# Performance work log

Measured on AMD Instinct MI355X. Metric: run time of the kernel, lower is better.

Reference implementation:

```python
import jax, jax.numpy as jnp
import numpy as np

N, G, E, F, H = 65536, 32768, 600000, 128, 128

def _mlp(x, w1, b1, w2, b2):
    # Linear -> SiLU -> Linear
    return jax.nn.silu(x @ w1 + b1) @ w2 + b2

def setup_inputs() -> dict:
    key = jax.random.key(0)
    ks = jax.random.split(key, 24)
    def lin(k, din, dout):
        kw, kb = jax.random.split(k)
        s = 1.0 / np.sqrt(din)
        return (jax.random.uniform(kw, (din, dout), jnp.float32, -s, s),
                jax.random.uniform(kb, (dout,), jnp.float32, -s, s))
    nm_w1, nm_b1 = lin(ks[0], F, H)
    nm_w2, nm_b2 = lin(ks[1], H, H)
    em_w1, em_b1 = lin(ks[2], 6, H)
    em_w2, em_b2 = lin(ks[3], H, H)
    mm_w1, mm_b1 = lin(ks[4], 2 * H, H)
    mm_w2, mm_b2 = lin(ks[5], H, H)
    um_w1, um_b1 = lin(ks[6], H, H)
    um_w2, um_b2 = lin(ks[7], H, H)
    return {
        "node_features": jax.random.normal(ks[8], (N, F), jnp.float32),
        "node_pos": jax.random.uniform(ks[9], (N, 3), jnp.float32),
        "grid_pos": jax.random.uniform(ks[10], (G, 3), jnp.float32),
        "edge_index": jax.random.randint(ks[11], (2, E), 0, G, jnp.int64),
        "nm_w1": nm_w1, "nm_b1": nm_b1, "nm_w2": nm_w2, "nm_b2": nm_b2,
        "em_w1": em_w1, "em_b1": em_b1, "em_w2": em_w2, "em_b2": em_b2,
        "mm_w1": mm_w1, "mm_b1": mm_b1, "mm_w2": mm_w2, "mm_b2": mm_b2,
        "um_w1": um_w1, "um_b1": um_b1, "um_w2": um_w2, "um_b2": um_b2,
    }

def reference(node_features, node_pos, grid_pos, edge_index,
              nm_w1, nm_b1, nm_w2, nm_b2,
              em_w1, em_b1, em_w2, em_b2,
              mm_w1, mm_b1, mm_w2, mm_b2,
              um_w1, um_b1, um_w2, um_b2):
    src, tgt = edge_index[0], edge_index[1]
    # node_model on all points [N,H]
    nf = _mlp(node_features, nm_w1, nm_b1, nm_w2, nm_b2)
    # edge features from gathered positions [E,6] -> [E,H]
    edge_attr = jnp.concatenate([node_pos[src], grid_pos[tgt]], axis=-1)
    ef = _mlp(edge_attr, em_w1, em_b1, em_w2, em_b2)
    # messages [E,2H] -> [E,H]
    msg = _mlp(jnp.concatenate([nf[src], ef], axis=-1), mm_w1, mm_b1, mm_w2, mm_b2)
    # scatter-add mean aggregation to grid [G,H]
    counts = jax.ops.segment_sum(jnp.ones((msg.shape[0],), msg.dtype), tgt, num_segments=G)
    counts = jnp.maximum(counts, 1.0)[:, None]
    agg = jax.ops.segment_sum(msg, tgt, num_segments=G) / counts
    # update_model [G,H]
    return _mlp(agg, um_w1, um_b1, um_w2, um_b2)
```

## Files before the change

kernel.cpp:

```cpp
#include <hip/hip_runtime.h>

#define N_NODES 65536
#define G_GRID  32768
#define E_EDGES 600000
#define HD      128

typedef __attribute__((ext_vector_type(8))) short bf8;
typedef __attribute__((ext_vector_type(4))) float f32x4;

__device__ __forceinline__ short f2bf(float f){
  union { float f; unsigned u; } v; v.f = f;
  unsigned r = v.u + 0x7FFFu + ((v.u >> 16) & 1u);
  return (short)(r >> 16);
}

__device__ __forceinline__ bf8 load_pack8(const float* p, float scale){
  float4 u0 = *(const float4*)p;
  float4 u1 = *(const float4*)(p + 4);
  bf8 r;
  r[0]=f2bf(u0.x*scale); r[1]=f2bf(u0.y*scale); r[2]=f2bf(u0.z*scale); r[3]=f2bf(u0.w*scale);
  r[4]=f2bf(u1.x*scale); r[5]=f2bf(u1.y*scale); r[6]=f2bf(u1.z*scale); r[7]=f2bf(u1.w*scale);
  return r;
}

__global__ void prep_w_k(const float* __restrict__ nmw1, const float* __restrict__ nmw2,
                         const float* __restrict__ emw2, const float* __restrict__ mmw1,
                         const float* __restrict__ mmw2, const float* __restrict__ umw1,
                         const float* __restrict__ umw2, short* __restrict__ dst)
{
  int i = blockIdx.x*256 + threadIdx.x;
  const float* src; int local; bool k256 = false;
  if      (i < 16384){ src = nmw1; local = i; }
  else if (i < 32768){ src = nmw2; local = i - 16384; }
  else if (i < 49152){ src = emw2; local = i - 32768; }
  else if (i < 81920){ src = mmw1; local = i - 49152; k256 = true; }
  else if (i < 98304){ src = mmw2; local = i - 81920; }
  else if (i < 114688){ src = umw1; local = i - 98304; }
  else               { src = umw2; local = i - 114688; }
  int n, k;
  if (k256){ n = local >> 8; k = local & 255; }
  else     { n = local >> 7; k = local & 127; }
  dst[i] = f2bf(src[k*HD + n]);
}

__global__ void prep_combo_k(const float* __restrict__ emw1, const float* __restrict__ eb1,
                             const float* __restrict__ emw2, const float* __restrict__ eb2,
                             const float* __restrict__ mmw1, const float* __restrict__ mb1,
                             short* __restrict__ wcombot, float* __restrict__ bcombo,
                             float* __restrict__ ew1c)
{
  int gid = blockIdx.x*256 + threadIdx.x;
  if (gid < 16384){
    int k = gid >> 7, n = gid & 127;
    float a0 = 0.f, a1 = 0.f;
    #pragma unroll 4
    for (int j=0;j<HD;j+=2){
      a0 += emw2[k*HD + j]     * mmw1[(HD + j)*HD + n];
      a1 += emw2[k*HD + j + 1] * mmw1[(HD + j + 1)*HD + n];
    }
    wcombot[n*HD + k] = f2bf(a0 + a1);
  } else if (gid < 16512){
    int n = gid - 16384;
    float acc = mb1[n];
    for (int j=0;j<HD;j++) acc += eb2[j] * mmw1[(HD + j)*HD + n];
    bcombo[n] = acc;
  } else if (gid < 16640){
    int n = gid - 16512;
    #pragma unroll
    for (int k=0;k<6;k++) ew1c[n*8 + k] = emw1[k*HD + n];
    ew1c[n*8 + 6] = eb1[n];
    ew1c[n*8 + 7] = 0.f;
  }
}

__global__ void node_mlp_k(const float* __restrict__ X,
                           const short* __restrict__ w1t, const float* __restrict__ b1,
                           const short* __restrict__ w2t, const float* __restrict__ b2,
                           short* __restrict__ nf)
{
  __shared__ short hid[64][136];
  const int t = threadIdx.x;
  const int wave = t >> 6, lane = t & 63, l15 = lane & 15, q = lane >> 4;
  const int rw = blockIdx.x*64 + wave*16;

  bf8 a[4];
  const float* xr = X + (size_t)(rw + l15)*HD;
  #pragma unroll
  for (int kt=0; kt<4; kt++) a[kt] = load_pack8(xr + kt*32 + q*8, 1.0f);

  #pragma unroll
  for (int ct=0; ct<8; ct++){
    f32x4 acc = {0.f,0.f,0.f,0.f};
    #pragma unroll
    for (int kt=0; kt<4; kt++){
      bf8 b = *(const bf8*)(w1t + (ct*16 + l15)*HD + kt*32 + q*8);
      acc = __builtin_amdgcn_mfma_f32_16x16x32_bf16(a[kt], b, acc, 0, 0, 0);
    }
    float bias = b1[ct*16 + l15];
    #pragma unroll
    for (int r=0;r<4;r++){
      float v = acc[r] + bias;
      v = v / (1.f + __expf(-v));
      hid[wave*16 + q*4 + r][ct*16 + l15] = f2bf(v);
    }
  }
  bf8 a2[4];
  #pragma unroll
  for (int kt=0;kt<4;kt++) a2[kt] = *(const bf8*)&hid[wave*16 + l15][kt*32 + q*8];
  #pragma unroll
  for (int ct=0; ct<8; ct++){
    f32x4 acc = {0.f,0.f,0.f,0.f};
    #pragma unroll
    for (int kt=0;kt<4;kt++){
      bf8 b = *(const bf8*)(w2t + (ct*16 + l15)*HD + kt*32 + q*8);
      acc = __builtin_amdgcn_mfma_f32_16x16x32_bf16(a2[kt], b, acc, 0, 0, 0);
    }
    float bias = b2[ct*16 + l15];
    #pragma unroll
    for (int r=0;r<4;r++)
      nf[(size_t)(rw + q*4 + r)*HD + ct*16 + l15] = f2bf(acc[r] + bias);
  }
}

__global__ void count_k(const int* __restrict__ eidx, int* __restrict__ counts){
  int e = blockIdx.x*256 + threadIdx.x;
  if (e < E_EDGES) atomicAdd(&counts[eidx[E_EDGES + e]], 1);
}

__global__ void scan_k(const int* __restrict__ counts, int* __restrict__ offs){
  __shared__ int part[1024];
  const int t = threadIdx.x;
  const int base = t*32;
  int loc[32];
  int s = 0;
  #pragma unroll
  for (int i=0;i<32;i++){ loc[i] = s; s += counts[base+i]; }
  part[t] = s;
  __syncthreads();
  for (int off=1; off<1024; off<<=1){
    int v = (t>=off) ? part[t-off] : 0;
    __syncthreads();
    part[t] += v;
    __syncthreads();
  }
  int pre = (t==0) ? 0 : part[t-1];
  #pragma unroll
  for (int i=0;i<32;i++) offs[base+i] = pre + loc[i];
  if (t==1023) offs[G_GRID] = pre + s;
}

__global__ void scatter_k(const int* __restrict__ eidx, const int* __restrict__ offs,
                          int* __restrict__ counts,
                          int* __restrict__ srcs_s, int* __restrict__ tgts_s){
  int e = blockIdx.x*256 + threadIdx.x;
  if (e < E_EDGES){
    int g = eidx[E_EDGES + e];
    int slot = offs[g] + atomicSub(&counts[g], 1) - 1;
    srcs_s[slot] = eidx[e];
    tgts_s[slot] = g;
  }
}

__global__ void __launch_bounds__(256, 3)
edge_msg5_k(const int* __restrict__ srcs_s, const int* __restrict__ tgts_s,
            const float* __restrict__ npos, const float* __restrict__ gpos,
            const float* __restrict__ ew1c_g, const float* __restrict__ bcombo,
            const short* __restrict__ mw1t, const short* __restrict__ wcombot,
            const short* __restrict__ mw2t, const float* __restrict__ mb2,
            const short* __restrict__ nf, float* __restrict__ agg)
{
  __shared__ float ew1l[128][8];
  __shared__ int tgtl[128];
  __shared__ short hm[128][136];

  const int t = threadIdx.x;
  const int e0 = blockIdx.x*128;
  const int w = t >> 6, lane = t & 63, l15 = lane & 15, q = lane >> 4;
  const int base = e0 + w*32;

  int i0 = base + l15;      if (i0 >= E_EDGES) i0 = E_EDGES - 1;
  int i1 = base + 16 + l15; if (i1 >= E_EDGES) i1 = E_EDGES - 1;
  int s0 = srcs_s[i0], s1 = srcs_s[i1];
  int g0 = tgts_s[i0], g1 = tgts_s[i1];

  bf8 an0[4], an1[4];
  {
    const short* n0p = nf + (size_t)s0*HD + q*8;
    const short* n1p = nf + (size_t)s1*HD + q*8;
    #pragma unroll
    for (int kt=0;kt<4;kt++){ an0[kt] = *(const bf8*)(n0p + kt*32); an1[kt] = *(const bf8*)(n1p + kt*32); }
  }
  float a0=npos[s0*3+0], a1=npos[s0*3+1], a2=npos[s0*3+2];
  float a3=gpos[g0*3+0], a4=gpos[g0*3+1], a5=gpos[g0*3+2];
  float b0=npos[s1*3+0], b1=npos[s1*3+1], b2=npos[s1*3+2];
  float b3=gpos[g1*3+0], b4=gpos[g1*3+1], b5=gpos[g1*3+2];

  if (t < 128){
    int idx = e0 + t; if (idx >= E_EDGES) idx = E_EDGES - 1;
    tgtl[t] = tgts_s[idx];
    *(f32x4*)&ew1l[t][0] = *(const f32x4*)&ew1c_g[t*8];
    *(f32x4*)&ew1l[t][4] = *(const f32x4*)&ew1c_g[t*8 + 4];
  }
  __syncthreads();

  {
    int r0 = w*32 + l15, r1 = r0 + 16;
    #pragma unroll
    for (int pg=0; pg<4; pg++){
      bf8 pk0, pk1;
      #pragma unroll
      for (int j=0;j<8;j++){
        int n = q*32 + pg*8 + j;
        f32x4 wa = *(const f32x4*)&ew1l[n][0];
        f32x4 wb = *(const f32x4*)&ew1l[n][4];
        float v0 = wb[2] + a0*wa[0] + a1*wa[1] + a2*wa[2] + a3*wa[3] + a4*wb[0] + a5*wb[1];
        v0 = v0 / (1.f + __expf(-v0));
        pk0[j] = f2bf(v0);
        float v1 = wb[2] + b0*wa[0] + b1*wa[1] + b2*wa[2] + b3*wa[3] + b4*wb[0] + b5*wb[1];
        v1 = v1 / (1.f + __expf(-v1));
        pk1[j] = f2bf(v1);
      }
      *(bf8*)&hm[r0][q*32 + pg*8] = pk0;
      *(bf8*)&hm[r1][q*32 + pg*8] = pk1;
    }
  }

  bf8 ah0[4], ah1[4];
  #pragma unroll
  for (int kt=0;kt<4;kt++){
    ah0[kt] = *(const bf8*)&hm[w*32 + l15][kt*32 + q*8];
    ah1[kt] = *(const bf8*)&hm[w*32 + 16 + l15][kt*32 + q*8];
  }
  #pragma unroll
  for (int ct=0; ct<8; ct++){
    bf8 bw1[4], bwc[4];
    #pragma unroll
    for (int kt=0;kt<4;kt++){
      bw1[kt] = *(const bf8*)(mw1t + (ct*16 + l15)*256 + kt*32 + q*8);
      bwc[kt] = *(const bf8*)(wcombot + (ct*16 + l15)*HD + kt*32 + q*8);
    }
    f32x4 acc0 = {0.f,0.f,0.f,0.f}, acc1 = {0.f,0.f,0.f,0.f};
    #pragma unroll
    for (int kt=0;kt<4;kt++){
      acc0 = __builtin_amdgcn_mfma_f32_16x16x32_bf16(an0[kt], bw1[kt], acc0, 0,0,0);
      acc1 = __builtin_amdgcn_mfma_f32_16x16x32_bf16(an1[kt], bw1[kt], acc1, 0,0,0);
    }
    #pragma unroll
    for (int kt=0;kt<4;kt++){
      acc0 = __builtin_amdgcn_mfma_f32_16x16x32_bf16(ah0[kt], bwc[kt], acc0, 0,0,0);
      acc1 = __builtin_amdgcn_mfma_f32_16x16x32_bf16(ah1[kt], bwc[kt], acc1, 0,0,0);
    }
    float bias = bcombo[ct*16 + l15];
    int col = ct*16 + l15;
    #pragma unroll
    for (int r=0;r<4;r++){
      float v0 = acc0[r] + bias;
      v0 = v0 / (1.f + __expf(-v0));
      hm[w*32 + q*4 + r][col] = f2bf(v0);
      float v1 = acc1[r] + bias;
      v1 = v1 / (1.f + __expf(-v1));
      hm[w*32 + 16 + q*4 + r][col] = f2bf(v1);
    }
  }

  bf8 am0[4], am1[4];
  #pragma unroll
  for (int kt=0;kt<4;kt++){
    am0[kt] = *(const bf8*)&hm[w*32 + l15][kt*32 + q*8];
    am1[kt] = *(const bf8*)&hm[w*32 + 16 + l15][kt*32 + q*8];
  }

  float* msgf_w = (float*)&hm[w*32][0];
  int lim0 = E_EDGES - base;      if (lim0 > 16) lim0 = 16;
  int lim1 = E_EDGES - base - 16; if (lim1 > 16) lim1 = 16;
  int c2 = lane*2;
  int cur = -1; float sx = 0.f, sy = 0.f;

  #pragma unroll
  for (int ct=0; ct<8; ct++){
    f32x4 acc = {0.f,0.f,0.f,0.f};
    #pragma unroll
    for (int kt=0;kt<4;kt++){
      bf8 b = *(const bf8*)(mw2t + (ct*16 + l15)*HD + kt*32 + q*8);
      acc = __builtin_amdgcn_mfma_f32_16x16x32_bf16(am0[kt], b, acc, 0,0,0);
    }
    float bias = mb2[ct*16 + l15];
    int col = ct*16 + l15;
    #pragma unroll
    for (int r=0;r<4;r++) msgf_w[(q*4 + r)*132 + col] = acc[r] + bias;
  }
  if (lim0 > 0){
    cur = tgtl[w*32];
    for (int r=0; r<lim0; r++){
      int tg = tgtl[w*32 + r];
      float2 v = *(const float2*)&msgf_w[r*132 + c2];
      if (tg != cur){
        atomicAdd(&agg[(size_t)cur*HD + c2], sx);
        atomicAdd(&agg[(size_t)cur*HD + c2 + 1], sy);
        cur = tg; sx = v.x; sy = v.y;
      } else { sx += v.x; sy += v.y; }
    }
  }

  if (lim1 > 0){
    #pragma unroll
    for (int ct=0; ct<8; ct++){
      f32x4 acc = {0.f,0.f,0.f,0.f};
      #pragma unroll
      for (int kt=0;kt<4;kt++){
        bf8 b = *(const bf8*)(mw2t + (ct*16 + l15)*HD + kt*32 + q*8);
        acc = __builtin_amdgcn_mfma_f32_16x16x32_bf16(am1[kt], b, acc, 0,0,0);
      }
      float bias = mb2[ct*16 + l15];
      int col = ct*16 + l15;
      #pragma unroll
      for (int r=0;r<4;r++) msgf_w[(q*4 + r)*132 + col] = acc[r] + bias;
    }
    for (int r=0; r<lim1; r++){
      int tg = tgtl[w*32 + 16 + r];
      float2 v = *(const float2*)&msgf_w[r*132 + c2];
      if (tg != cur){
        atomicAdd(&agg[(size_t)cur*HD + c2], sx);
        atomicAdd(&agg[(size_t)cur*HD + c2 + 1], sy);
        cur = tg; sx = v.x; sy = v.y;
      } else { sx += v.x; sy += v.y; }
    }
  }
  if (cur >= 0){
    atomicAdd(&agg[(size_t)cur*HD + c2], sx);
    atomicAdd(&agg[(size_t)cur*HD + c2 + 1], sy);
  }
}

__global__ void update_mlp2_k(const float* __restrict__ agg, const int* __restrict__ offs,
                              const short* __restrict__ w1t, const float* __restrict__ b1,
                              const short* __restrict__ w2t, const float* __restrict__ b2,
                              float* __restrict__ out)
{
  __shared__ short hid[64][136];
  const int t = threadIdx.x;
  const int wave = t >> 6, lane = t & 63, l15 = lane & 15, q = lane >> 4;
  const int rw = blockIdx.x*64 + wave*16;

  int row = rw + l15;
  float c = (float)(offs[row+1] - offs[row]);
  float rcp = 1.0f / fmaxf(c, 1.0f);
  bf8 a[4];
  const float* ar = agg + (size_t)row*HD;
  #pragma unroll
  for (int kt=0; kt<4; kt++) a[kt] = load_pack8(ar + kt*32 + q*8, rcp);

  #pragma unroll
  for (int ct=0; ct<8; ct++){
    f32x4 acc = {0.f,0.f,0.f,0.f};
    #pragma unroll
    for (int kt=0; kt<4; kt++){
      bf8 b = *(const bf8*)(w1t + (ct*16 + l15)*HD + kt*32 + q*8);
      acc = __builtin_amdgcn_mfma_f32_16x16x32_bf16(a[kt], b, acc, 0, 0, 0);
    }
    float bias = b1[ct*16 + l15];
    #pragma unroll
    for (int r=0;r<4;r++){
      float v = acc[r] + bias;
      v = v / (1.f + __expf(-v));
      hid[wave*16 + q*4 + r][ct*16 + l15] = f2bf(v);
    }
  }
  bf8 a2[4];
  #pragma unroll
  for (int kt=0;kt<4;kt++) a2[kt] = *(const bf8*)&hid[wave*16 + l15][kt*32 + q*8];
  #pragma unroll
  for (int ct=0; ct<8; ct++){
    f32x4 acc = {0.f,0.f,0.f,0.f};
    #pragma unroll
    for (int kt=0;kt<4;kt++){
      bf8 b = *(const bf8*)(w2t + (ct*16 + l15)*HD + kt*32 + q*8);
      acc = __builtin_amdgcn_mfma_f32_16x16x32_bf16(a2[kt], b, acc, 0, 0, 0);
    }
    float bias = b2[ct*16 + l15];
    #pragma unroll
    for (int r=0;r<4;r++)
      out[(size_t)(rw + q*4 + r)*HD + ct*16 + l15] = acc[r] + bias;
  }
}

extern "C" void kernel_launch(void* const* d_in, const int* in_sizes, int n_in,
                              void* d_out, int out_size, void* d_ws, size_t ws_size,
                              hipStream_t stream)
{
  const float* node_features = (const float*)d_in[0];
  const float* node_pos      = (const float*)d_in[1];
  const float* grid_pos      = (const float*)d_in[2];
  const int*   edge_index    = (const int*)d_in[3];
  const float* nm_w1 = (const float*)d_in[4];
  const float* nm_b1 = (const float*)d_in[5];
  const float* nm_w2 = (const float*)d_in[6];
  const float* nm_b2 = (const float*)d_in[7];
  const float* em_w1 = (const float*)d_in[8];
  const float* em_b1 = (const float*)d_in[9];
  const float* em_w2 = (const float*)d_in[10];
  const float* em_b2 = (const float*)d_in[11];
  const float* mm_w1 = (const float*)d_in[12];
  const float* mm_b1 = (const float*)d_in[13];
  const float* mm_w2 = (const float*)d_in[14];
  const float* mm_b2 = (const float*)d_in[15];
  const float* um_w1 = (const float*)d_in[16];
  const float* um_b1 = (const float*)d_in[17];
  const float* um_w2 = (const float*)d_in[18];
  const float* um_b2 = (const float*)d_in[19];
  float* out = (float*)d_out;

  char* ws = (char*)d_ws;
  short* nf     = (short*)ws;
  int*   counts = (int*)  (ws + 16777216ull);
  int*   offs   = (int*)  (ws + 16908288ull);
  short* wts    = (short*)(ws + 17039424ull);
  short* wcombot= (short*)(ws + 17301568ull);
  float* bcombo = (float*)(ws + 17334336ull);
  float* ew1c   = (float*)(ws + 17334848ull);
  int*   srcs_s = (int*)  (ws + 17338944ull);
  int*   tgts_s = (int*)  (ws + 19738944ull);

  short* nmw1t = wts;
  short* nmw2t = wts + 16384;
  short* mmw1t = wts + 49152;
  short* mmw2t = wts + 81920;
  short* umw1t = wts + 98304;
  short* umw2t = wts + 114688;

  float* agg = out;

  (void)hipMemsetAsync(counts, 0, 131072, stream);
  (void)hipMemsetAsync(out, 0, (size_t)G_GRID*HD*4, stream);

  prep_w_k<<<512, 256, 0, stream>>>(nm_w1, nm_w2, em_w2, mm_w1, mm_w2, um_w1, um_w2, wts);
  prep_combo_k<<<65, 256, 0, stream>>>(em_w1, em_b1, em_w2, em_b2, mm_w1, mm_b1,
                                       wcombot, bcombo, ew1c);
  node_mlp_k<<<G_GRID/64, 256, 0, stream>>>(node_features, nmw1t, nm_b1, nmw2t, nm_b2, nf);
  count_k<<<(E_EDGES+255)/256, 256, 0, stream>>>(edge_index, counts);
  scan_k<<<1, 1024, 0, stream>>>(counts, offs);
  scatter_k<<<(E_EDGES+255)/256, 256, 0, stream>>>(edge_index, offs, counts, srcs_s, tgts_s);
  edge_msg5_k<<<(E_EDGES + 127)/128, 256, 0, stream>>>(srcs_s, tgts_s, node_pos, grid_pos,
      ew1c, bcombo, mmw1t, wcombot, mmw2t, mm_b2, nf, agg);
  update_mlp2_k<<<G_GRID/64, 256, 0, stream>>>(agg, offs, umw1t, um_b1, umw2t, um_b2, out);
}
```

Baseline: 538.7 us.

## Compute edge-MLP first layer with split-bf16 MFMA instead of scalar FMAs

The 6-input first edge-MLP layer now runs on MFMA instead of per-lane scalar FMA loops over an LDS weight table. Inputs and weights are split into hi/lo bf16 parts and packed into a K=32 fragment with a constant-one bias column, so fp32 accuracy is roughly kept (hi*hi + lo*hi + hi*lo terms). This removes the LDS weight staging and a block-wide barrier. The weight-combination prep kernel is also split across more blocks with a two-half reduction. The cost is extra packing work per edge and a more scattered write pattern into the shared hidden tile.

```diff
diff --git a/kernel.cpp b/kernel.cpp
--- a/kernel.cpp
+++ b/kernel.cpp
@@ -12,6 +12,9 @@
   union { float f; unsigned u; } v; v.f = f;
   unsigned r = v.u + 0x7FFFu + ((v.u >> 16) & 1u);
   return (short)(r >> 16);
+}
+__device__ __forceinline__ float bf2f(short s){
+  union { unsigned u; float f; } v; v.u = ((unsigned)(unsigned short)s) << 16; return v.f;
 }
 
 __device__ __forceinline__ bf8 load_pack8(const float* p, float scale){
@@ -43,33 +46,46 @@
   dst[i] = f2bf(src[k*HD + n]);
 }
 
-__global__ void prep_combo_k(const float* __restrict__ emw1, const float* __restrict__ eb1,
-                             const float* __restrict__ emw2, const float* __restrict__ eb2,
-                             const float* __restrict__ mmw1, const float* __restrict__ mb1,
-                             short* __restrict__ wcombot, float* __restrict__ bcombo,
-                             float* __restrict__ ew1c)
-{
-  int gid = blockIdx.x*256 + threadIdx.x;
-  if (gid < 16384){
-    int k = gid >> 7, n = gid & 127;
-    float a0 = 0.f, a1 = 0.f;
-    #pragma unroll 4
-    for (int j=0;j<HD;j+=2){
-      a0 += emw2[k*HD + j]     * mmw1[(HD + j)*HD + n];
-      a1 += emw2[k*HD + j + 1] * mmw1[(HD + j + 1)*HD + n];
-    }
-    wcombot[n*HD + k] = f2bf(a0 + a1);
-  } else if (gid < 16512){
-    int n = gid - 16384;
-    float acc = mb1[n];
-    for (int j=0;j<HD;j++) acc += eb2[j] * mmw1[(HD + j)*HD + n];
-    bcombo[n] = acc;
-  } else if (gid < 16640){
-    int n = gid - 16512;
-    #pragma unroll
-    for (int k=0;k<6;k++) ew1c[n*8 + k] = emw1[k*HD + n];
-    ew1c[n*8 + 6] = eb1[n];
-    ew1c[n*8 + 7] = 0.f;
+__global__ void prep_combo2_k(const float* __restrict__ emw1, const float* __restrict__ eb1,
+                              const float* __restrict__ emw2, const float* __restrict__ eb2,
+                              const float* __restrict__ mmw1, const float* __restrict__ mb1,
+                              short* __restrict__ wcombot, float* __restrict__ bcombo,
+                              short* __restrict__ ew1x)
+{
+  if (blockIdx.x < 128){
+    __shared__ float part[2][128];
+    int k = blockIdx.x;
+    int t = threadIdx.x, n = t & 127, half = t >> 7;
+    float acc = 0.f;
+    const float* er = emw2 + k*HD + half*64;
+    #pragma unroll 8
+    for (int j=0;j<64;j++) acc += er[j] * mmw1[(HD + half*64 + j)*HD + n];
+    part[half][n] = acc;
+    __syncthreads();
+    if (half == 0) wcombot[n*HD + k] = f2bf(part[0][n] + part[1][n]);
+  } else {
+    int t = threadIdx.x;
+    if (t < 128){
+      int n = t;
+      float acc = mb1[n];
+      for (int j=0;j<HD;j++) acc += eb2[j] * mmw1[(HD + j)*HD + n];
+      bcombo[n] = acc;
+      short v[32];
+      #pragma unroll
+      for (int i=0;i<32;i++) v[i] = 0;
+      #pragma unroll
+      for (int i=0;i<6;i++){
+        float wv = emw1[i*HD + n];
+        short wh = f2bf(wv);
+        short wl = f2bf(wv - bf2f(wh));
+        v[i] = wh; v[6+i] = wh; v[12+i] = wl;
+      }
+      float bv = eb1[n];
+      short bh = f2bf(bv);
+      v[18] = bh; v[19] = f2bf(bv - bf2f(bh));
+      #pragma unroll
+      for (int i=0;i<32;i++) ew1x[n*32 + i] = v[i];
+    }
   }
 }
 
@@ -161,15 +177,34 @@
   }
 }
 
+__device__ __forceinline__ bf8 build_af(const float p[6], int q){
+  short ph[6], pl[6];
+  #pragma unroll
+  for (int i=0;i<6;i++){
+    ph[i] = f2bf(p[i]);
+    pl[i] = f2bf(p[i] - bf2f(ph[i]));
+  }
+  bf8 af = {0,0,0,0,0,0,0,0};
+  if (q == 0){
+    af[0]=ph[0]; af[1]=ph[1]; af[2]=ph[2]; af[3]=ph[3];
+    af[4]=ph[4]; af[5]=ph[5]; af[6]=pl[0]; af[7]=pl[1];
+  } else if (q == 1){
+    af[0]=pl[2]; af[1]=pl[3]; af[2]=pl[4]; af[3]=pl[5];
+    af[4]=ph[0]; af[5]=ph[1]; af[6]=ph[2]; af[7]=ph[3];
+  } else if (q == 2){
+    af[0]=ph[4]; af[1]=ph[5]; af[2]=(short)0x3F80; af[3]=(short)0x3F80;
+  }
+  return af;
+}
+
 __global__ void __launch_bounds__(256, 3)
-edge_msg5_k(const int* __restrict__ srcs_s, const int* __restrict__ tgts_s,
+edge_msg6_k(const int* __restrict__ srcs_s, const int* __restrict__ tgts_s,
             const float* __restrict__ npos, const float* __restrict__ gpos,
-            const float* __restrict__ ew1c_g, const float* __restrict__ bcombo,
+            const short* __restrict__ ew1x, const float* __restrict__ bcombo,
             const short* __restrict__ mw1t, const short* __restrict__ wcombot,
             const short* __restrict__ mw2t, const float* __restrict__ mb2,
             const short* __restrict__ nf, float* __restrict__ agg)
 {
-  __shared__ float ew1l[128][8];
   __shared__ int tgtl[128];
   __shared__ short hm[128][136];
 
@@ -190,38 +225,34 @@
     #pragma unroll
     for (int kt=0;kt<4;kt++){ an0[kt] = *(const bf8*)(n0p + kt*32); an1[kt] = *(const bf8*)(n1p + kt*32); }
   }
-  float a0=npos[s0*3+0], a1=npos[s0*3+1], a2=npos[s0*3+2];
-  float a3=gpos[g0*3+0], a4=gpos[g0*3+1], a5=gpos[g0*3+2];
-  float b0=npos[s1*3+0], b1=npos[s1*3+1], b2=npos[s1*3+2];
-  float b3=gpos[g1*3+0], b4=gpos[g1*3+1], b5=gpos[g1*3+2];
-
-  if (t < 128){
-    int idx = e0 + t; if (idx >= E_EDGES) idx = E_EDGES - 1;
-    tgtl[t] = tgts_s[idx];
-    *(f32x4*)&ew1l[t][0] = *(const f32x4*)&ew1c_g[t*8];
-    *(f32x4*)&ew1l[t][4] = *(const f32x4*)&ew1c_g[t*8 + 4];
-  }
-  __syncthreads();
-
-  {
-    int r0 = w*32 + l15, r1 = r0 + 16;
-    #pragma unroll
-    for (int pg=0; pg<4; pg++){
-      bf8 pk0, pk1;
-      #pragma unroll
-      for (int j=0;j<8;j++){
-        int n = q*32 + pg*8 + j;
-        f32x4 wa = *(const f32x4*)&ew1l[n][0];
-        f32x4 wb = *(const f32x4*)&ew1l[n][4];
-        float v0 = wb[2] + a0*wa[0] + a1*wa[1] + a2*wa[2] + a3*wa[3] + a4*wb[0] + a5*wb[1];
-        v0 = v0 / (1.f + __expf(-v0));
-        pk0[j] = f2bf(v0);
-        float v1 = wb[2] + b0*wa[0] + b1*wa[1] + b2*wa[2] + b3*wa[3] + b4*wb[0] + b5*wb[1];
-        v1 = v1 / (1.f + __expf(-v1));
-        pk1[j] = f2bf(v1);
-      }
-      *(bf8*)&hm[r0][q*32 + pg*8] = pk0;
-      *(bf8*)&hm[r1][q*32 + pg*8] = pk1;
+  float pA[6], pB[6];
+  pA[0]=npos[s0*3+0]; pA[1]=npos[s0*3+1]; pA[2]=npos[s0*3+2];
+  pA[3]=gpos[g0*3+0]; pA[4]=gpos[g0*3+1]; pA[5]=gpos[g0*3+2];
+  pB[0]=npos[s1*3+0]; pB[1]=npos[s1*3+1]; pB[2]=npos[s1*3+2];
+  pB[3]=gpos[g1*3+0]; pB[4]=gpos[g1*3+1]; pB[5]=gpos[g1*3+2];
+
+  if (lane < 32){
+    int idx = base + lane; if (idx >= E_EDGES) idx = E_EDGES - 1;
+    tgtl[w*32 + lane] = tgts_s[idx];
+  }
+
+  bf8 af0 = build_af(pA, q);
+  bf8 af1 = build_af(pB, q);
+  #pragma unroll
+  for (int ct=0; ct<8; ct++){
+    bf8 bw = *(const bf8*)(ew1x + (ct*16 + l15)*32 + q*8);
+    f32x4 h0 = {0.f,0.f,0.f,0.f}, h1 = {0.f,0.f,0.f,0.f};
+    h0 = __builtin_amdgcn_mfma_f32_16x16x32_bf16(af0, bw, h0, 0,0,0);
+    h1 = __builtin_amdgcn_mfma_f32_16x16x32_bf16(af1, bw, h1, 0,0,0);
+    int col = ct*16 + l15;
+    #pragma unroll
+    for (int r=0;r<4;r++){
+      float v0 = h0[r];
+      v0 = v0 / (1.f + __expf(-v0));
+      hm[w*32 + q*4 + r][col] = f2bf(v0);
+      float v1 = h1[r];
+      v1 = v1 / (1.f + __expf(-v1));
+      hm[w*32 + 16 + q*4 + r][col] = f2bf(v1);
     }
   }
 
@@ -417,9 +448,9 @@
   short* wts    = (short*)(ws + 17039424ull);
   short* wcombot= (short*)(ws + 17301568ull);
   float* bcombo = (float*)(ws + 17334336ull);
-  float* ew1c   = (float*)(ws + 17334848ull);
-  int*   srcs_s = (int*)  (ws + 17338944ull);
-  int*   tgts_s = (int*)  (ws + 19738944ull);
+  short* ew1x   = (short*)(ws + 17334848ull);
+  int*   srcs_s = (int*)  (ws + 17343040ull);
+  int*   tgts_s = (int*)  (ws + 19743040ull);
 
   short* nmw1t = wts;
   short* nmw2t = wts + 16384;
@@ -434,13 +465,13 @@
   (void)hipMemsetAsync(out, 0, (size_t)G_GRID*HD*4, stream);
 
   prep_w_k<<<512, 256, 0, stream>>>(nm_w1, nm_w2, em_w2, mm_w1, mm_w2, um_w1, um_w2, wts);
-  prep_combo_k<<<65, 256, 0, stream>>>(em_w1, em_b1, em_w2, em_b2, mm_w1, mm_b1,
-                                       wcombot, bcombo, ew1c);
+  prep_combo2_k<<<129, 256, 0, stream>>>(em_w1, em_b1, em_w2, em_b2, mm_w1, mm_b1,
+                                         wcombot, bcombo, ew1x);
   node_mlp_k<<<G_GRID/64, 256, 0, stream>>>(node_features, nmw1t, nm_b1, nmw2t, nm_b2, nf);
   count_k<<<(E_EDGES+255)/256, 256, 0, stream>>>(edge_index, counts);
   scan_k<<<1, 1024, 0, stream>>>(counts, offs);
   scatter_k<<<(E_EDGES+255)/256, 256, 0, stream>>>(edge_index, offs, counts, srcs_s, tgts_s);
-  edge_msg5_k<<<(E_EDGES + 127)/128, 256, 0, stream>>>(srcs_s, tgts_s, node_pos, grid_pos,
-      ew1c, bcombo, mmw1t, wcombot, mmw2t, mm_b2, nf, agg);
+  edge_msg6_k<<<(E_EDGES + 127)/128, 256, 0, stream>>>(srcs_s, tgts_s, node_pos, grid_pos,
+      ew1x, bcombo, mmw1t, wcombot, mmw2t, mm_b2, nf, agg);
   update_mlp2_k<<<G_GRID/64, 256, 0, stream>>>(agg, offs, umw1t, um_b1, umw2t, um_b2, out);
 }
```

Result: no change. 543.4 us (+0.9%).
